# Kernel tuning notes

Measured on AMD Instinct MI355X. Metric: run time of the kernel, lower is better.

Reference implementation:

```python
import jax, jax.numpy as jnp
import numpy as np

V = 1024          # vocab (blank index = V, output size V+1)
B, T, U = 4, 256, 64
ENC_D, PRED_H, JOINT_D = 512, 640, 640


def setup_inputs() -> dict:
    key = jax.random.key(0)
    ks = jax.random.split(key, 16)
    s = 0.02
    return {
        "encoder_output": jax.random.normal(ks[0], (B, ENC_D, T), jnp.float32),
        "encoder_lengths": jax.random.randint(ks[1], (B,), T // 2, T + 1, jnp.int32),
        "targets": jax.random.randint(ks[2], (B, U), 0, V, jnp.int32),
        "target_lengths": jax.random.randint(ks[3], (B,), U // 2, U + 1, jnp.int32),
        # prediction network params (Embedding + LSTM, torch gate order i,f,g,o)
        "embed": jax.random.normal(ks[4], (V + 1, PRED_H), jnp.float32) * s,
        "w_ih": jax.random.normal(ks[5], (4 * PRED_H, PRED_H), jnp.float32) * s,
        "w_hh": jax.random.normal(ks[6], (4 * PRED_H, PRED_H), jnp.float32) * s,
        "b_ih": jnp.zeros((4 * PRED_H,), jnp.float32),
        "b_hh": jnp.zeros((4 * PRED_H,), jnp.float32),
        # joint params
        "enc_w": jax.random.normal(ks[7], (JOINT_D, ENC_D), jnp.float32) * s,
        "enc_b": jnp.zeros((JOINT_D,), jnp.float32),
        "pred_w": jax.random.normal(ks[8], (JOINT_D, PRED_H), jnp.float32) * s,
        "pred_b": jnp.zeros((JOINT_D,), jnp.float32),
        "out_w": jax.random.normal(ks[9], (V + 1, JOINT_D), jnp.float32) * s,
        "out_b": jnp.zeros((V + 1,), jnp.float32),
    }


def _lstm(y, w_ih, w_hh, b_ih, b_hh):
    # y: [B, L, H] -> hidden states [B, L, H]
    h0 = jnp.zeros((y.shape[0], w_hh.shape[1]), y.dtype)
    c0 = h0

    def step(carry, xt):
        h, c = carry
        gates = xt @ w_ih.T + h @ w_hh.T + b_ih + b_hh
        i, f, g, o = jnp.split(gates, 4, axis=-1)
        c = jax.nn.sigmoid(f) * c + jax.nn.sigmoid(i) * jnp.tanh(g)
        h = jax.nn.sigmoid(o) * jnp.tanh(c)
        return (h, c), h

    _, hs = jax.lax.scan(step, (h0, c0), jnp.swapaxes(y, 0, 1))  # [L, B, H]
    return jnp.swapaxes(hs, 0, 1)


def reference(encoder_output, encoder_lengths, targets, target_lengths,
              embed, w_ih, w_hh, b_ih, b_hh,
              enc_w, enc_b, pred_w, pred_b, out_w, out_b):
    # prediction network: embed targets, prepend SOS (zero vector), LSTM
    y = embed[targets]                                        # [B, U, H]
    sos = jnp.zeros((y.shape[0], 1, y.shape[2]), y.dtype)
    y = jnp.concatenate([sos, y], axis=1)                     # [B, U+1, H]
    pred = _lstm(y, w_ih, w_hh, b_ih, b_hh)                   # [B, U+1, H]

    enc = jnp.swapaxes(encoder_output, 1, 2)                  # [B, T, D]
    f_enc = enc @ enc_w.T + enc_b                             # [B, T, J]
    f_pred = pred @ pred_w.T + pred_b                         # [B, U+1, J]
    joint = jax.nn.relu(f_enc[:, :, None, :] + f_pred[:, None, :, :])  # [B,T,U+1,J]
    logits = joint @ out_w.T + out_b                          # [B,T,U+1,V+1]
    return logits
```

## Files before the change

kernel.cpp:

```cpp
#include <hip/hip_runtime.h>
#include <hip/hip_bf16.h>
#include <hip/hip_cooperative_groups.h>
#include <cstddef>
#include <cstdint>


#define BB 4
#define TT 256
#define U1 65
#define HH 640
#define G4 2560
#define ED 512
#define JJ 640
#define V1 1025
#define MROWS (BB*TT*U1)

typedef __attribute__((ext_vector_type(8))) short bf16x8;
typedef __attribute__((ext_vector_type(4))) float f32x4;

#define GLOAD_LDS16(g, s) __builtin_amdgcn_global_load_lds( \
    (const __attribute__((address_space(1))) void*)(g), \
    (__attribute__((address_space(3))) void*)(s), 16, 0, 0)

__device__ __forceinline__ float sigm(float x) { return 1.f / (1.f + expf(-x)); }

__global__ __launch_bounds__(256) void transpose_tiled(const float* __restrict__ in,
                                                       float* __restrict__ out,
                                                       int R, int C) {
    __shared__ float t[32][33];
    const int bx = blockIdx.x * 32;
    const int by = blockIdx.y * 32;
    const int x = threadIdx.x & 31;
    const int y0 = threadIdx.x >> 5;
#pragma unroll
    for (int i = 0; i < 32; i += 8)
        t[y0 + i][x] = in[(size_t)(by + y0 + i) * C + bx + x];
    __syncthreads();
#pragma unroll
    for (int i = 0; i < 32; i += 8)
        out[(size_t)(bx + y0 + i) * R + by + x] = t[x][y0 + i];
}

__global__ __launch_bounds__(256) void build_y(const int* __restrict__ tgt,
                                               const float* __restrict__ embed,
                                               float* __restrict__ y) {
    int idx = blockIdx.x * 256 + threadIdx.x;
    if (idx >= BB * U1 * HH) return;
    int h = idx % HH;
    int bu = idx / HH;
    int u = bu % U1, b = bu / U1;
    y[idx] = (u == 0) ? 0.f : embed[(size_t)tgt[b * 64 + (u - 1)] * HH + h];
}

__global__ __launch_bounds__(256) void gemm_x(const float* __restrict__ y,
                                              const float* __restrict__ w_ihT,
                                              const float* __restrict__ b_ih,
                                              const float* __restrict__ b_hh,
                                              float* __restrict__ X) {
    __shared__ float ys[4][HH];
    int cg = blockIdx.x % 10;
    int rg = blockIdx.x / 10;
    int row = cg * 256 + threadIdx.x;
    for (int e = threadIdx.x; e < 4 * HH / 4; e += 256)
        ((float4*)ys)[e] = ((const float4*)(y + (size_t)rg * 4 * HH))[e];
    __syncthreads();
    float bias = b_ih[row] + b_hh[row];
    float a0 = bias, a1 = bias, a2 = bias, a3 = bias;
#pragma unroll 8
    for (int k = 0; k < HH; k++) {
        float w = w_ihT[(size_t)k * G4 + row];
        a0 += ys[0][k] * w;
        a1 += ys[1][k] * w;
        a2 += ys[2][k] * w;
        a3 += ys[3][k] * w;
    }
    X[(size_t)(rg * 4 + 0) * G4 + row] = a0;
    X[(size_t)(rg * 4 + 1) * G4 + row] = a1;
    X[(size_t)(rg * 4 + 2) * G4 + row] = a2;
    X[(size_t)(rg * 4 + 3) * G4 + row] = a3;
}

__global__ __launch_bounds__(256) void lstm_all(const float* __restrict__ X,
                                                const float* __restrict__ w_hhT,
                                                float* __restrict__ pred) {
    int b = blockIdx.x / 20;
    int chunk = blockIdx.x % 20;
    __shared__ float hs[HH];
    __shared__ float part[8][128];
    __shared__ float gl[128];
    const int tid = threadIdx.x;
    const int q = tid & 31;
    const int ksl = tid >> 5;
    const int g = q >> 3, jq = q & 7;
    const int grow = g * HH + chunk * 32 + jq * 4;
    const float4* w4 = (const float4*)w_hhT;
    const int w4idx0 = grow >> 2;
    const int rowX = (tid >> 5) * HH + chunk * 32 + (tid & 31);
    float creg = 0.f;
    cooperative_groups::grid_group grid = cooperative_groups::this_grid();

    for (int s = 0; s < U1; s++) {
        float xv = 0.f;
        if (tid < 128) xv = X[(size_t)(b * U1 + s) * G4 + rowX];
        if (tid < 160) {
            ((float4*)hs)[tid] = (s == 0) ? (float4){0.f, 0.f, 0.f, 0.f}
                : ((const float4*)(pred + (size_t)(b * U1 + (s - 1)) * HH))[tid];
        }
        __syncthreads();
        float4 acc = {0.f, 0.f, 0.f, 0.f};
        const int k0 = ksl * 80;
#pragma unroll 8
        for (int k = 0; k < 80; k++) {
            float h = hs[k0 + k];
            float4 w = w4[(size_t)(k0 + k) * (G4 / 4) + w4idx0];
            acc.x += h * w.x; acc.y += h * w.y; acc.z += h * w.z; acc.w += h * w.w;
        }
        *(float4*)&part[ksl][q * 4] = acc;
        __syncthreads();
        if (tid < 128) {
            float sum = 0.f;
#pragma unroll
            for (int i = 0; i < 8; i++) sum += part[i][tid];
            gl[tid] = sum + xv;
        }
        __syncthreads();
        if (tid < 32) {
            float iv = sigm(gl[0 * 32 + tid]);
            float fv = sigm(gl[1 * 32 + tid]);
            float gv = tanhf(gl[2 * 32 + tid]);
            float ov = sigm(gl[3 * 32 + tid]);
            creg = fv * creg + iv * gv;
            float h = ov * tanhf(creg);
            pred[(size_t)(b * U1 + s) * HH + chunk * 32 + tid] = h;
        }
        grid.sync();
    }
}

__global__ __launch_bounds__(256) void fenc_k(const float* __restrict__ encT,
                                              const float* __restrict__ enc_wT,
                                              const float* __restrict__ enc_b,
                                              float* __restrict__ fenc) {
    __shared__ float es[4][ED];
    int r0 = blockIdx.x * 4;
    for (int e = threadIdx.x; e < 4 * ED / 4; e += 256)
        ((float4*)es)[e] = ((const float4*)(encT + (size_t)r0 * ED))[e];
    __syncthreads();
    for (int j = threadIdx.x; j < JJ; j += 256) {
        float bias = enc_b[j];
        float a0 = bias, a1 = bias, a2 = bias, a3 = bias;
#pragma unroll 8
        for (int d = 0; d < ED; d++) {
            float w = enc_wT[(size_t)d * JJ + j];
            a0 += es[0][d] * w;
            a1 += es[1][d] * w;
            a2 += es[2][d] * w;
            a3 += es[3][d] * w;
        }
        fenc[(size_t)(r0 + 0) * JJ + j] = a0;
        fenc[(size_t)(r0 + 1) * JJ + j] = a1;
        fenc[(size_t)(r0 + 2) * JJ + j] = a2;
        fenc[(size_t)(r0 + 3) * JJ + j] = a3;
    }
}

__global__ __launch_bounds__(256) void fpred_k(const float* __restrict__ pred,
                                               const float* __restrict__ pred_wT,
                                               const float* __restrict__ pred_b,
                                               float* __restrict__ fpred) {
    __shared__ float ps[4][HH];
    int r0 = blockIdx.x * 4;
    for (int e = threadIdx.x; e < 4 * HH / 4; e += 256)
        ((float4*)ps)[e] = ((const float4*)(pred + (size_t)r0 * HH))[e];
    __syncthreads();
    for (int j = threadIdx.x; j < JJ; j += 256) {
        float bias = pred_b[j];
        float a0 = bias, a1 = bias, a2 = bias, a3 = bias;
#pragma unroll 8
        for (int k = 0; k < HH; k++) {
            float w = pred_wT[(size_t)k * JJ + j];
            a0 += ps[0][k] * w;
            a1 += ps[1][k] * w;
            a2 += ps[2][k] * w;
            a3 += ps[3][k] * w;
        }
        fpred[(size_t)(r0 + 0) * JJ + j] = a0;
        fpred[(size_t)(r0 + 1) * JJ + j] = a1;
        fpred[(size_t)(r0 + 2) * JJ + j] = a2;
        fpred[(size_t)(r0 + 3) * JJ + j] = a3;
    }
}

__global__ __launch_bounds__(256) void cvt_bf16_k(const float4* __restrict__ in,
                                                  ushort4* __restrict__ outp, int n4) {
    int i = blockIdx.x * 256 + threadIdx.x;
    if (i >= n4) return;
    float4 v = in[i];
    ushort4 o;
    __hip_bfloat16 h0 = __float2bfloat16(v.x);
    __hip_bfloat16 h1 = __float2bfloat16(v.y);
    __hip_bfloat16 h2 = __float2bfloat16(v.z);
    __hip_bfloat16 h3 = __float2bfloat16(v.w);
    o.x = *(ushort*)&h0; o.y = *(ushort*)&h1;
    o.z = *(ushort*)&h2; o.w = *(ushort*)&h3;
    outp[i] = o;
}

__global__ __launch_bounds__(256) void joint_mfma(const float* __restrict__ fenc,
                                                  const float* __restrict__ fpred,
                                                  const __hip_bfloat16* __restrict__ W,
                                                  const float* __restrict__ out_b,
                                                  float* __restrict__ out) {
    __shared__ __align__(16) short Abuf[2][4096];
    __shared__ __align__(16) short Bbuf[2][4096];
    const int lin = blockIdx.y * 9 + blockIdx.x;
    const int swz = (lin & 7) * 585 + (lin >> 3);
    const int v0 = (swz % 9) * 128;
    const int row0 = (swz / 9) * 128;
    const int tid = threadIdx.x;
    const int l = tid & 63;
    const int wv = tid >> 6;
    const int wr = wv >> 1, wc = wv & 1;

    const char* Wb = (const char*)W;
    const int brow = v0 + wv * 32 + (l >> 2);
    const int ksegB = (l & 3) * 16;

    const int arow_l = tid >> 1;
    const int kh = tid & 1;
    const int am = row0 + arow_l;
    const int abt = am / 65;
    const int au = am - abt * 65;
    const int ab = abt >> 8;
    const float* feP = fenc + (size_t)abt * JJ + kh * 16;
    const float* fpP = fpred + (size_t)(ab * U1 + au) * JJ + kh * 16;

    f32x4 acc[4][4];
#pragma unroll
    for (int i = 0; i < 4; i++)
#pragma unroll
        for (int j = 0; j < 4; j++) acc[i][j] = (f32x4){0.f, 0.f, 0.f, 0.f};

    auto stageW = [&](int buf, int kc) {
        size_t kb = (size_t)kc * 64;
#pragma unroll
        for (int i = 0; i < 2; i++) {
            int vr = brow + i * 16;
            if (vr > 1024) vr = 1024;
            const char* g = Wb + (size_t)vr * 1280 + kb + ksegB;
            GLOAD_LDS16(g, &Bbuf[buf][wv * 1024 + i * 512]);
        }
    };
    auto stageA = [&](int buf, int kc) {
        const int k0 = kc * 32;
        float4 e0 = *(const float4*)(feP + k0);
        float4 e1 = *(const float4*)(feP + k0 + 4);
        float4 e2 = *(const float4*)(feP + k0 + 8);
        float4 e3 = *(const float4*)(feP + k0 + 12);
        float4 p0 = *(const float4*)(fpP + k0);
        float4 p1 = *(const float4*)(fpP + k0 + 4);
        float4 p2 = *(const float4*)(fpP + k0 + 8);
        float4 p3 = *(const float4*)(fpP + k0 + 12);
        float v[16] = {
            e0.x + p0.x, e0.y + p0.y, e0.z + p0.z, e0.w + p0.w,
            e1.x + p1.x, e1.y + p1.y, e1.z + p1.z, e1.w + p1.w,
            e2.x + p2.x, e2.y + p2.y, e2.z + p2.z, e2.w + p2.w,
            e3.x + p3.x, e3.y + p3.y, e3.z + p3.z, e3.w + p3.w};
        union { ushort h[16]; uint4 q[2]; } pk;
#pragma unroll
        for (int i = 0; i < 16; i++) {
            __hip_bfloat16 hb = __float2bfloat16(fmaxf(v[i], 0.f));
            pk.h[i] = *(ushort*)&hb;
        }
        *(uint4*)&Abuf[buf][arow_l * 32 + kh * 16] = pk.q[0];
        *(uint4*)&Abuf[buf][arow_l * 32 + kh * 16 + 8] = pk.q[1];
    };

    stageW(0, 0);
    stageA(0, 0);
    int cur = 0;
    const int lr = l & 15, lg = l >> 4;
    for (int kc = 0; kc < 20; kc++) {
        __syncthreads();
        if (kc < 19) stageW(cur ^ 1, kc + 1);
        bf16x8 af[4], bfr[4];
#pragma unroll
        for (int mf = 0; mf < 4; mf++)
            af[mf] = *(const bf16x8*)&Abuf[cur][(wr * 64 + mf * 16 + lr) * 32 + lg * 8];
#pragma unroll
        for (int nf = 0; nf < 4; nf++)
            bfr[nf] = *(const bf16x8*)&Bbuf[cur][(wc * 64 + nf * 16 + lr) * 32 + lg * 8];
#pragma unroll
        for (int mf = 0; mf < 4; mf++)
#pragma unroll
            for (int nf = 0; nf < 4; nf++)
                acc[mf][nf] = __builtin_amdgcn_mfma_f32_16x16x32_bf16(af[mf], bfr[nf], acc[mf][nf], 0, 0, 0);
        if (kc < 19) stageA(cur ^ 1, kc + 1);
        cur ^= 1;
    }

#pragma unroll
    for (int nf = 0; nf < 4; nf++) {
        int vcol = v0 + wc * 64 + nf * 16 + lr;
        if (vcol < V1) {
            float bias = out_b[vcol];
#pragma unroll
            for (int mf = 0; mf < 4; mf++) {
#pragma unroll
                for (int rg = 0; rg < 4; rg++) {
                    int m = row0 + wr * 64 + mf * 16 + lg * 4 + rg;
                    out[(size_t)m * V1 + vcol] = acc[mf][nf][rg] + bias;
                }
            }
        }
    }
}

extern "C" void kernel_launch(void* const* d_in, const int* in_sizes, int n_in,
                              void* d_out, int out_size, void* d_ws, size_t ws_size,
                              hipStream_t stream) {
    const float* enc = (const float*)d_in[0];
    const int* targets = (const int*)d_in[2];
    const float* embed = (const float*)d_in[4];
    const float* w_ih = (const float*)d_in[5];
    const float* w_hh = (const float*)d_in[6];
    const float* b_ih = (const float*)d_in[7];
    const float* b_hh = (const float*)d_in[8];
    const float* enc_w = (const float*)d_in[9];
    const float* enc_b = (const float*)d_in[10];
    const float* pred_w = (const float*)d_in[11];
    const float* pred_b = (const float*)d_in[12];
    const float* out_w = (const float*)d_in[13];
    const float* out_b = (const float*)d_in[14];
    float* out = (float*)d_out;

    float* w0 = (float*)d_ws;
    size_t o = 0;
    float* w_ihT = w0 + o; o += (size_t)640 * 2560;
    float* w_hhT = w0 + o; o += (size_t)640 * 2560;
    float* enc_wT = w0 + o; o += (size_t)512 * 640;
    float* pred_wT = w0 + o; o += (size_t)640 * 640;
    float* encT = w0 + o; o += (size_t)BB * TT * ED;
    float* y = w0 + o; o += (size_t)BB * U1 * HH;
    float* X = w0 + o; o += (size_t)BB * U1 * G4;
    float* pred = w0 + o; o += (size_t)BB * U1 * HH;
    float* fenc = w0 + o; o += (size_t)BB * TT * JJ;
    float* fpred = w0 + o; o += (size_t)BB * U1 * JJ;
    __hip_bfloat16* W_bf = (__hip_bfloat16*)(w0 + o); o += (size_t)V1 * JJ / 2 + 8;

    auto TP = [&](const float* in, float* outp, int R, int C) {
        transpose_tiled<<<dim3(C / 32, R / 32), 256, 0, stream>>>(in, outp, R, C);
    };
    TP(w_ih, w_ihT, 2560, 640);
    TP(w_hh, w_hhT, 2560, 640);
    TP(enc_w, enc_wT, 640, 512);
    TP(pred_w, pred_wT, 640, 640);
    for (int b = 0; b < BB; b++)
        TP(enc + (size_t)b * ED * TT, encT + (size_t)b * TT * ED, ED, TT);

    build_y<<<(BB * U1 * HH + 255) / 256, 256, 0, stream>>>(targets, embed, y);
    gemm_x<<<650, 256, 0, stream>>>(y, w_ihT, b_ih, b_hh, X);

    {
        void* kargs[] = {(void*)&X, (void*)&w_hhT, (void*)&pred};
        hipLaunchCooperativeKernel((void*)lstm_all, dim3(80), dim3(256), kargs, 0, stream);
    }

    fenc_k<<<BB * TT / 4, 256, 0, stream>>>(encT, enc_wT, enc_b, fenc);
    fpred_k<<<BB * U1 / 4, 256, 0, stream>>>(pred, pred_wT, pred_b, fpred);
    cvt_bf16_k<<<(V1 * JJ / 4 + 255) / 256, 256, 0, stream>>>((const float4*)out_w,
                                                              (ushort4*)W_bf, V1 * JJ / 4);
    joint_mfma<<<dim3(9, 520), 256, 0, stream>>>(fenc, fpred, W_bf, out_b, out);
}
```

Baseline: 2.018 ms.

## Replace LSTM grid-wide sync with per-batch atomic counters and prefetch joint A loads

Drops the cooperative grid.sync in the LSTM recurrence. Each batch's 20 blocks now signal step completion through a per-(batch,step) atomic counter, and consumers spin on it, so batches no longer wait on each other and the full-grid barrier cost goes away. The joint MFMA kernel also splits its A staging into a global load issued before the MFMAs and a convert-and-store after them, overlapping the load latency with compute. The LSTM inner loop unroll goes from 8 to 16. This adds a small zeroing kernel and relies on relaxed atomics plus release ordering for correctness, and spinning needs all blocks co-resident.

```diff
diff --git a/kernel.cpp b/kernel.cpp
--- a/kernel.cpp
+++ b/kernel.cpp
@@ -39,6 +39,11 @@
 #pragma unroll
     for (int i = 0; i < 32; i += 8)
         out[(size_t)(bx + y0 + i) * R + by + x] = t[x][y0 + i];
+}
+
+__global__ __launch_bounds__(256) void zero_cnt(int* __restrict__ cnt) {
+    int i = blockIdx.x * 256 + threadIdx.x;
+    if (i < BB * U1) cnt[i] = 0;
 }
 
 __global__ __launch_bounds__(256) void build_y(const int* __restrict__ tgt,
@@ -82,7 +87,8 @@
 
 __global__ __launch_bounds__(256) void lstm_all(const float* __restrict__ X,
                                                 const float* __restrict__ w_hhT,
-                                                float* __restrict__ pred) {
+                                                float* __restrict__ pred,
+                                                int* __restrict__ cnt) {
     int b = blockIdx.x / 20;
     int chunk = blockIdx.x % 20;
     __shared__ float hs[HH];
@@ -97,19 +103,33 @@
     const int w4idx0 = grow >> 2;
     const int rowX = (tid >> 5) * HH + chunk * 32 + (tid & 31);
     float creg = 0.f;
-    cooperative_groups::grid_group grid = cooperative_groups::this_grid();
 
     for (int s = 0; s < U1; s++) {
         float xv = 0.f;
         if (tid < 128) xv = X[(size_t)(b * U1 + s) * G4 + rowX];
-        if (tid < 160) {
-            ((float4*)hs)[tid] = (s == 0) ? (float4){0.f, 0.f, 0.f, 0.f}
-                : ((const float4*)(pred + (size_t)(b * U1 + (s - 1)) * HH))[tid];
+        if (s == 0) {
+            if (tid < 160) ((float4*)hs)[tid] = (float4){0.f, 0.f, 0.f, 0.f};
+        } else {
+            if (tid == 0) {
+                while (__hip_atomic_load(&cnt[b * U1 + s - 1], __ATOMIC_RELAXED,
+                                         __HIP_MEMORY_SCOPE_AGENT) < 20)
+                    __builtin_amdgcn_s_sleep(1);
+            }
+            __syncthreads();
+            if (tid < 160) {
+                float* hp = pred + (size_t)(b * U1 + (s - 1)) * HH + tid * 4;
+                float4 v;
+                v.x = __hip_atomic_load(hp + 0, __ATOMIC_RELAXED, __HIP_MEMORY_SCOPE_AGENT);
+                v.y = __hip_atomic_load(hp + 1, __ATOMIC_RELAXED, __HIP_MEMORY_SCOPE_AGENT);
+                v.z = __hip_atomic_load(hp + 2, __ATOMIC_RELAXED, __HIP_MEMORY_SCOPE_AGENT);
+                v.w = __hip_atomic_load(hp + 3, __ATOMIC_RELAXED, __HIP_MEMORY_SCOPE_AGENT);
+                ((float4*)hs)[tid] = v;
+            }
         }
         __syncthreads();
         float4 acc = {0.f, 0.f, 0.f, 0.f};
         const int k0 = ksl * 80;
-#pragma unroll 8
+#pragma unroll 16
         for (int k = 0; k < 80; k++) {
             float h = hs[k0 + k];
             float4 w = w4[(size_t)(k0 + k) * (G4 / 4) + w4idx0];
@@ -131,9 +151,13 @@
             float ov = sigm(gl[3 * 32 + tid]);
             creg = fv * creg + iv * gv;
             float h = ov * tanhf(creg);
-            pred[(size_t)(b * U1 + s) * HH + chunk * 32 + tid] = h;
-        }
-        grid.sync();
+            __hip_atomic_store(&pred[(size_t)(b * U1 + s) * HH + chunk * 32 + tid], h,
+                               __ATOMIC_RELAXED, __HIP_MEMORY_SCOPE_AGENT);
+        }
+        __syncthreads();
+        if (tid == 0)
+            __hip_atomic_fetch_add(&cnt[b * U1 + s], 1, __ATOMIC_RELEASE,
+                                   __HIP_MEMORY_SCOPE_AGENT);
     }
 }
 
@@ -251,21 +275,26 @@
             GLOAD_LDS16(g, &Bbuf[buf][wv * 1024 + i * 512]);
         }
     };
-    auto stageA = [&](int buf, int kc) {
+    struct ARegs { float4 e0, e1, e2, e3, p0, p1, p2, p3; };
+    auto stageA_load = [&](int kc) -> ARegs {
         const int k0 = kc * 32;
-        float4 e0 = *(const float4*)(feP + k0);
-        float4 e1 = *(const float4*)(feP + k0 + 4);
-        float4 e2 = *(const float4*)(feP + k0 + 8);
-        float4 e3 = *(const float4*)(feP + k0 + 12);
-        float4 p0 = *(const float4*)(fpP + k0);
-        float4 p1 = *(const float4*)(fpP + k0 + 4);
-        float4 p2 = *(const float4*)(fpP + k0 + 8);
-        float4 p3 = *(const float4*)(fpP + k0 + 12);
+        ARegs r;
+        r.e0 = *(const float4*)(feP + k0);
+        r.e1 = *(const float4*)(feP + k0 + 4);
+        r.e2 = *(const float4*)(feP + k0 + 8);
+        r.e3 = *(const float4*)(feP + k0 + 12);
+        r.p0 = *(const float4*)(fpP + k0);
+        r.p1 = *(const float4*)(fpP + k0 + 4);
+        r.p2 = *(const float4*)(fpP + k0 + 8);
+        r.p3 = *(const float4*)(fpP + k0 + 12);
+        return r;
+    };
+    auto stageA_store = [&](int buf, const ARegs& r) {
         float v[16] = {
-            e0.x + p0.x, e0.y + p0.y, e0.z + p0.z, e0.w + p0.w,
-            e1.x + p1.x, e1.y + p1.y, e1.z + p1.z, e1.w + p1.w,
-            e2.x + p2.x, e2.y + p2.y, e2.z + p2.z, e2.w + p2.w,
-            e3.x + p3.x, e3.y + p3.y, e3.z + p3.z, e3.w + p3.w};
+            r.e0.x + r.p0.x, r.e0.y + r.p0.y, r.e0.z + r.p0.z, r.e0.w + r.p0.w,
+            r.e1.x + r.p1.x, r.e1.y + r.p1.y, r.e1.z + r.p1.z, r.e1.w + r.p1.w,
+            r.e2.x + r.p2.x, r.e2.y + r.p2.y, r.e2.z + r.p2.z, r.e2.w + r.p2.w,
+            r.e3.x + r.p3.x, r.e3.y + r.p3.y, r.e3.z + r.p3.z, r.e3.w + r.p3.w};
         union { ushort h[16]; uint4 q[2]; } pk;
 #pragma unroll
         for (int i = 0; i < 16; i++) {
@@ -277,12 +306,16 @@
     };
 
     stageW(0, 0);
-    stageA(0, 0);
+    stageA_store(0, stageA_load(0));
     int cur = 0;
     const int lr = l & 15, lg = l >> 4;
     for (int kc = 0; kc < 20; kc++) {
         __syncthreads();
-        if (kc < 19) stageW(cur ^ 1, kc + 1);
+        ARegs ar;
+        if (kc < 19) {
+            stageW(cur ^ 1, kc + 1);
+            ar = stageA_load(kc + 1);
+        }
         bf16x8 af[4], bfr[4];
 #pragma unroll
         for (int mf = 0; mf < 4; mf++)
@@ -295,7 +328,7 @@
 #pragma unroll
             for (int nf = 0; nf < 4; nf++)
                 acc[mf][nf] = __builtin_amdgcn_mfma_f32_16x16x32_bf16(af[mf], bfr[nf], acc[mf][nf], 0, 0, 0);
-        if (kc < 19) stageA(cur ^ 1, kc + 1);
+        if (kc < 19) stageA_store(cur ^ 1, ar);
         cur ^= 1;
     }
 
@@ -347,6 +380,7 @@
     float* fenc = w0 + o; o += (size_t)BB * TT * JJ;
     float* fpred = w0 + o; o += (size_t)BB * U1 * JJ;
     __hip_bfloat16* W_bf = (__hip_bfloat16*)(w0 + o); o += (size_t)V1 * JJ / 2 + 8;
+    int* cnt = (int*)(w0 + o); o += BB * U1;
 
     auto TP = [&](const float* in, float* outp, int R, int C) {
         transpose_tiled<<<dim3(C / 32, R / 32), 256, 0, stream>>>(in, outp, R, C);
@@ -358,11 +392,12 @@
     for (int b = 0; b < BB; b++)
         TP(enc + (size_t)b * ED * TT, encT + (size_t)b * TT * ED, ED, TT);
 
+    zero_cnt<<<2, 256, 0, stream>>>(cnt);
     build_y<<<(BB * U1 * HH + 255) / 256, 256, 0, stream>>>(targets, embed, y);
     gemm_x<<<650, 256, 0, stream>>>(y, w_ihT, b_ih, b_hh, X);
 
     {
-        void* kargs[] = {(void*)&X, (void*)&w_hhT, (void*)&pred};
+        void* kargs[] = {(void*)&X, (void*)&w_hhT, (void*)&pred, (void*)&cnt};
         hipLaunchCooperativeKernel((void*)lstm_all, dim3(80), dim3(256), kargs, 0, stream);
     }
 
```

Measured after the change: 1.637 ms. 18.9% less time.
